# Performance work log

Measured on AMD Instinct MI355X. Metric: run time of the kernel, lower is better.

The kernel has to match this reference:

```python
import jax, jax.numpy as jnp
import numpy as np


def setup_inputs() -> dict:
    key = jax.random.key(0)
    k1, k2, k3, k4 = jax.random.split(key, 4)
    b, h, t, dim, topk = 16, 8, 196, 512, 49
    x = jax.random.normal(k1, (b, t, dim), dtype=jnp.float32)
    adj = jax.random.normal(k2, (b, h, t, t), dtype=jnp.float32)  # per-head routing logits
    Wqkv = jax.random.normal(k3, (dim, 3 * dim), dtype=jnp.float32) * 0.02
    Wv = jax.random.normal(k4, (dim, dim), dtype=jnp.float32) * 0.02
    return {"x": x, "adj": adj, "Wqkv": Wqkv, "Wv": Wv, "topk": topk}


def reference(x, adj, Wqkv, Wv, topk):
    b, t, dim = x.shape
    h = adj.shape[1]
    d = dim // h
    scale = dim ** (-0.5)  # note: full dim, matching source (self.scale = dim**-0.5)

    # qkv projection (stand-in for GIN conv_proj_qkv with nhid = 3*dim)
    qkv = (x @ Wqkv).reshape(b, t, h, 3 * d).transpose(0, 2, 1, 3)  # b h t 3d
    q, k, v = jnp.split(qkv, 3, axis=-1)  # each b h t d

    # TopkRouting: indices of top-k routing logits per (b, h, query-token)
    _, r_idx = jax.lax.top_k(adj, topk)  # b h t topk (r_weight unused: mul_weight='none')

    # KGather: irregular gather of concatenated k/v rows per query token
    kv = jnp.concatenate([k, v], axis=-1).reshape(b * h, t, 2 * d)
    idx = r_idx.reshape(b * h, t, topk)
    kv_sel = jax.vmap(lambda m, i: m[i])(kv, idx)          # (bh, t, topk, 2d)
    kv_sel = kv_sel.reshape(b, h, t, topk, 2 * d)
    k_sel, v_sel = jnp.split(kv_sel, 2, axis=-1)            # b h t topk d

    # small-window attention: each query attends to its topk gathered rows (w^2 = 1)
    attn = jax.nn.softmax(jnp.einsum('bhtd,bhtkd->bhtk', q * scale, k_sel), axis=-1)
    o = jnp.einsum('bhtk,bhtkd->bhtd', attn, v_sel)

    o = o.transpose(0, 2, 1, 3).reshape(b, t, dim)
    o = jax.nn.gelu(o, approximate=False)  # torch F.gelu default = exact erf
    return o @ Wv
```

## Files before the change

### kernel.cpp

```cpp
#include <hip/hip_runtime.h>
#include <hip/hip_bf16.h>
#include <cmath>

#define B_   16
#define H_   8
#define T_   196
#define DIM_ 512
#define DHEAD_ 64
#define TOPK_ 49
#define BT_  (B_ * T_)
#define BH_  (B_ * H_)

#define QB_OFF   0u
#define KB_OFF   1605632u
#define VT_OFF   3211264u
#define XB_OFF   5046272u
#define WQKVT_OFF 6651904u
#define WVT_OFF  7438336u
#define MASK_OFF 7700480u

typedef __bf16 bf16x8 __attribute__((ext_vector_type(8)));
typedef float f32x4 __attribute__((ext_vector_type(4)));

__device__ __forceinline__ unsigned short f2bf(float f) {
    union { float f; unsigned int u; } v; v.f = f;
    const unsigned int u = v.u;
    return (unsigned short)((u + 0x7FFFu + ((u >> 16) & 1u)) >> 16);
}

__device__ __forceinline__ unsigned int ordered_u32(float f) {
    int i = __float_as_int(f);
    return (i < 0) ? ~(unsigned int)i : ((unsigned int)i | 0x80000000u);
}

__global__ __launch_bounds__(256) void prep_route(const float* __restrict__ x,
                                                  const float* __restrict__ adj,
                                                  const float* __restrict__ Wqkv,
                                                  const float* __restrict__ Wv,
                                                  unsigned short* __restrict__ xb,
                                                  unsigned short* __restrict__ wqkvT,
                                                  unsigned short* __restrict__ wvT,
                                                  unsigned short* __restrict__ vT,
                                                  unsigned int* __restrict__ masks) {
    __shared__ unsigned short Tt[64][72];
    const int t = threadIdx.x;
    const int bid = blockIdx.x;

    if (bid < 6272) {
        const int lane = t & 63;
        const int wid = t >> 6;
        const int q = bid * 4 + wid;
        const float* arow = adj + (size_t)q * T_;

        const bool v3 = (lane < 4);
        unsigned int u[4];
        u[0] = ordered_u32(arow[lane]);
        u[1] = ordered_u32(arow[lane + 64]);
        u[2] = ordered_u32(arow[lane + 128]);
        u[3] = v3 ? ordered_u32(arow[lane + 192]) : 0u;

        unsigned int prefix = 0u, thr = 0u;
        int k = TOPK_, A = T_;
        for (int b = 31; b >= 0; --b) {
            int C1 = 0;
            C1 += __popcll(__ballot(((u[0] ^ prefix) >> b) == 1u));
            C1 += __popcll(__ballot(((u[1] ^ prefix) >> b) == 1u));
            C1 += __popcll(__ballot(((u[2] ^ prefix) >> b) == 1u));
            C1 += __popcll(__ballot(((u[3] ^ prefix) >> b) == 1u));
            if (C1 >= k) { prefix |= (1u << b); A = C1; }
            else { k -= C1; A -= C1; }

            if (k == A || k == 1) {
                const bool mx = (k == 1);
                unsigned int best = mx ? 0u : 0xFFFFFFFFu;
#pragma unroll
                for (int s = 0; s < 4; ++s) {
                    const bool valid = (s < 3) || v3;
                    const bool act = valid && (((u[s] ^ prefix) >> b) == 0u);
                    if (act) best = mx ? (u[s] > best ? u[s] : best)
                                       : (u[s] < best ? u[s] : best);
                }
#pragma unroll
                for (int off = 32; off >= 1; off >>= 1) {
                    const unsigned int o = __shfl_xor(best, off);
                    best = mx ? (o > best ? o : best) : (o < best ? o : best);
                }
                thr = best;
                break;
            }
            if (b == 0) thr = prefix;
        }

        const unsigned long long lmask = (1ull << lane) - 1ull;
        unsigned long long gm[4];
        int G = 0;
#pragma unroll
        for (int s = 0; s < 4; ++s) {
            const bool valid = (s < 3) || v3;
            gm[s] = __ballot(valid && (u[s] > thr));
            G += __popcll(gm[s]);
        }
        const int need = TOPK_ - G;
        int cum = 0;
        unsigned long long sb0 = 0, sb1 = 0, sb2 = 0, sb3 = 0;
#pragma unroll
        for (int s = 0; s < 4; ++s) {
            const bool valid = (s < 3) || v3;
            const bool e = valid && (u[s] == thr);
            const unsigned long long em = __ballot(e);
            const int rk = cum + __popcll(em & lmask);
            cum += __popcll(em);
            const unsigned long long sel = gm[s] | __ballot(e && (rk < need));
            if (s == 0) sb0 = sel; else if (s == 1) sb1 = sel;
            else if (s == 2) sb2 = sel; else sb3 = sel;
        }
        if (lane < 8) {
            const unsigned long long mv = (lane < 2) ? sb0 : (lane < 4) ? sb1
                                        : (lane < 6) ? sb2 : sb3;
            const unsigned int wd = (lane & 1) ? (unsigned int)(mv >> 32) : (unsigned int)mv;
            masks[(size_t)q * 8 + lane] = wd;
        }
        return;
    }

    if (bid < 7056) {
        const size_t base = ((size_t)(bid - 6272) * 256 + t) * 8;
        const float4 v0 = *(const float4*)&x[base];
        const float4 v1 = *(const float4*)&x[base + 4];
        uint4 pk;
        pk.x = (unsigned int)f2bf(v0.x) | ((unsigned int)f2bf(v0.y) << 16);
        pk.y = (unsigned int)f2bf(v0.z) | ((unsigned int)f2bf(v0.w) << 16);
        pk.z = (unsigned int)f2bf(v1.x) | ((unsigned int)f2bf(v1.y) << 16);
        pk.w = (unsigned int)f2bf(v1.z) | ((unsigned int)f2bf(v1.w) << 16);
        *(uint4*)&xb[base] = pk;
        return;
    }
    if (bid >= 7312) {
        const int e0 = (bid - 7312) * 8192 + t;
#pragma unroll
        for (int i = 0; i < 32; ++i) {
            const int e = e0 + i * 256;
            const int bh = e / 1792;
            const int rem = e - bh * 1792;
            const int d = rem / 28;
            const int tt = rem - d * 28;
            vT[(size_t)bh * (64 * 224) + (size_t)d * 224 + 196 + tt] = 0;
        }
        return;
    }

    const float* src;
    unsigned short* dst;
    int Cc, R, tx, ty;
    if (bid < 7248) {
        const int b = bid - 7056;
        src = Wqkv; dst = wqkvT; Cc = 1536; R = 512; tx = b % 24; ty = b / 24;
    } else {
        const int b = bid - 7248;
        src = Wv; dst = wvT; Cc = 512; R = 512; tx = b % 8; ty = b / 8;
    }
    const int c0 = tx * 64;
    const int r0 = ty * 64;

#pragma unroll
    for (int p = 0; p < 4; ++p) {
        const int r = (t >> 4) + 16 * p;
        const int cl = (t & 15) * 4;
        const float4 v = *(const float4*)&src[(size_t)(r0 + r) * Cc + c0 + cl];
        Tt[cl + 0][r] = f2bf(v.x);
        Tt[cl + 1][r] = f2bf(v.y);
        Tt[cl + 2][r] = f2bf(v.z);
        Tt[cl + 3][r] = f2bf(v.w);
    }
    __syncthreads();
#pragma unroll
    for (int p = 0; p < 2; ++p) {
        const int cc = (t >> 3) + 32 * p;
        const int ch = (t & 7) * 8;
        const uint4 v = *(const uint4*)&Tt[cc][ch];
        *(uint4*)&dst[(size_t)(c0 + cc) * R + r0 + ch] = v;
    }
}

template <int BN, int MODE, typename CT>
__global__ __launch_bounds__(256) void gemm_mfma(const unsigned short* __restrict__ A,
                                                 const unsigned short* __restrict__ Bt,
                                                 CT* __restrict__ C,
                                                 const int M, const int N, const int K) {
    constexpr int FN = BN / 32;
    __shared__ unsigned short As[64][56];
    __shared__ unsigned short Bs[BN][56];
    __shared__ unsigned short Cs[(MODE == 1) ? 64 * 132 : 4];

    const int tid = threadIdx.x;
    const int lane = tid & 63, wid = tid >> 6;
    const int wr = wid >> 1, wc = wid & 1;
    const int row0 = blockIdx.x * 64;
    const int col0 = blockIdx.y * BN;

    f32x4 acc[2][FN];
#pragma unroll
    for (int m = 0; m < 2; ++m)
#pragma unroll
        for (int n = 0; n < FN; ++n)
            acc[m][n] = (f32x4){0.0f, 0.0f, 0.0f, 0.0f};

    const int ar = tid >> 2;
    const int ac = (tid & 3) * 8;
    const int fr = lane & 15;
    const int fk = (lane >> 4) * 8;

    for (int k0 = 0; k0 < K; k0 += 32) {
        *(uint4*)&As[ar][ac] = *(const uint4*)&A[(size_t)(row0 + ar) * K + k0 + ac];
#pragma unroll
        for (int p = 0; p < BN / 64; ++p)
            *(uint4*)&Bs[p * 64 + ar][ac] =
                *(const uint4*)&Bt[(size_t)(col0 + p * 64 + ar) * K + k0 + ac];
        __syncthreads();

        bf16x8 af[2], bfv[FN];
#pragma unroll
        for (int m = 0; m < 2; ++m)
            af[m] = *(const bf16x8*)&As[wr * 32 + m * 16 + fr][fk];
#pragma unroll
        for (int n = 0; n < FN; ++n)
            bfv[n] = *(const bf16x8*)&Bs[wc * (BN / 2) + n * 16 + fr][fk];
#pragma unroll
        for (int m = 0; m < 2; ++m)
#pragma unroll
            for (int n = 0; n < FN; ++n)
                acc[m][n] = __builtin_amdgcn_mfma_f32_16x16x32_bf16(af[m], bfv[n], acc[m][n], 0, 0, 0);
        __syncthreads();
    }

    if (MODE == 0) {
#pragma unroll
        for (int m = 0; m < 2; ++m)
#pragma unroll
            for (int n = 0; n < FN; ++n)
#pragma unroll
                for (int i = 0; i < 4; ++i) {
                    const int row = row0 + wr * 32 + m * 16 + (lane >> 4) * 4 + i;
                    const int col = col0 + wc * (BN / 2) + n * 16 + (lane & 15);
                    C[(size_t)row * N + col] = (CT)acc[m][n][i];
                }
    } else {
#pragma unroll
        for (int m = 0; m < 2; ++m)
#pragma unroll
            for (int n = 0; n < FN; ++n)
#pragma unroll
                for (int i = 0; i < 4; ++i) {
                    const int rl = wr * 32 + m * 16 + (lane >> 4) * 4 + i;
                    const int cl = wc * (BN / 2) + n * 16 + (lane & 15);
                    Cs[rl * 132 + cl] = f2bf(acc[m][n][i]);
                }
        __syncthreads();

        unsigned short* ubase = (unsigned short*)C;
#pragma unroll
        for (int ch = 0; ch < BN / 64; ++ch) {
            const int abscol = col0 + ch * 64;
            const int which = (abscol >> 6) % 3;
            const int hh = abscol / 192;
            if (which < 2) {
                const int r = tid >> 2;
                const int co = (tid & 3) * 16;
                const int gr = row0 + r;
                const int bb = gr / T_;
                const int tt = gr - bb * T_;
                const uint2 a0 = *(const uint2*)&Cs[r * 132 + ch * 64 + co];
                const uint2 a1 = *(const uint2*)&Cs[r * 132 + ch * 64 + co + 4];
                const uint2 a2 = *(const uint2*)&Cs[r * 132 + ch * 64 + co + 8];
                const uint2 a3 = *(const uint2*)&Cs[r * 132 + ch * 64 + co + 12];
                unsigned short* dst = ubase + (size_t)which * KB_OFF +
                                      ((size_t)(bb * H_ + hh) * T_ + tt) * DHEAD_ + co;
                uint4 w0; w0.x = a0.x; w0.y = a0.y; w0.z = a1.x; w0.w = a1.y;
                uint4 w1; w1.x = a2.x; w1.y = a2.y; w1.z = a3.x; w1.w = a3.y;
                *(uint4*)&dst[0] = w0;
                *(uint4*)&dst[8] = w1;
            } else {
                const int d = tid >> 2;
                const int j0 = (tid & 3) * 16;
                union { unsigned short s[16]; uint2 v2[4]; } tmp;
#pragma unroll
                for (int j = 0; j < 16; ++j)
                    tmp.s[j] = Cs[(j0 + j) * 132 + ch * 64 + d];
                const int gr0 = row0 + j0;
                const int bb0 = gr0 / T_;
                const int bb1 = (gr0 + 15) / T_;
                if (bb0 == bb1) {
                    const int tt = gr0 - bb0 * T_;
                    unsigned short* dst = ubase + VT_OFF +
                                          (size_t)(bb0 * H_ + hh) * (64 * 224) +
                                          (size_t)d * 224 + tt;
                    *(uint2*)&dst[0]  = tmp.v2[0];
                    *(uint2*)&dst[4]  = tmp.v2[1];
                    *(uint2*)&dst[8]  = tmp.v2[2];
                    *(uint2*)&dst[12] = tmp.v2[3];
                } else {
#pragma unroll
                    for (int j = 0; j < 16; ++j) {
                        const int gr = gr0 + j;
                        const int bb = gr / T_;
                        const int tt = gr - bb * T_;
                        ubase[VT_OFF + (size_t)(bb * H_ + hh) * (64 * 224) +
                              (size_t)d * 224 + tt] = tmp.s[j];
                    }
                }
            }
        }
    }
}

__global__ __launch_bounds__(256) void attn_mfma(const unsigned short* __restrict__ qb,
                                                 const unsigned short* __restrict__ kb,
                                                 const unsigned short* __restrict__ vT,
                                                 const unsigned int* __restrict__ masks,
                                                 unsigned short* __restrict__ obuf) {
    __shared__ unsigned int mask_lds[64][8];
    __shared__ unsigned short P[64][232];

    const int lane = threadIdx.x & 63;
    const int w = threadIdx.x >> 6;
    const int qt = blockIdx.x;
    const int bh = blockIdx.y;
    const int bb = bh >> 3, hh = bh & 7;
    const int q0 = qt * 64;

    for (int it = threadIdx.x; it < 512; it += 256) {
        const int r = it >> 3, wd = it & 7;
        const int t = q0 + r;
        mask_lds[r][wd] = (t < T_) ? masks[((size_t)bh * T_ + t) * 8 + wd] : 0u;
    }
    *(unsigned long long*)&P[threadIdx.x >> 2][208 + (threadIdx.x & 3) * 4] = 0ull;
    __syncthreads();

    const int fr = lane & 15;
    const int fk8 = (lane >> 4) * 8;
    const unsigned short* qbh = qb + ((size_t)bh * T_ + q0 + w * 16) * DHEAD_;
    const unsigned short* kbh = kb + (size_t)bh * T_ * DHEAD_;

    bf16x8 aq0 = *(const bf16x8*)&qbh[fr * 64 + fk8];
    bf16x8 aq1 = *(const bf16x8*)&qbh[fr * 64 + 32 + fk8];

    f32x4 s[13];
#pragma unroll
    for (int c = 0; c < 13; ++c) s[c] = (f32x4){0.0f, 0.0f, 0.0f, 0.0f};
#pragma unroll
    for (int c = 0; c < 13; ++c) {
        const bf16x8 b0 = *(const bf16x8*)&kbh[(c * 16 + fr) * 64 + fk8];
        const bf16x8 b1 = *(const bf16x8*)&kbh[(c * 16 + fr) * 64 + 32 + fk8];
        s[c] = __builtin_amdgcn_mfma_f32_16x16x32_bf16(aq0, b0, s[c], 0, 0, 0);
        s[c] = __builtin_amdgcn_mfma_f32_16x16x32_bf16(aq1, b1, s[c], 0, 0, 0);
    }

    const float scale = 0.044194173824159216f;
    float l0 = 0, l1 = 0, l2 = 0, l3 = 0;
#pragma unroll
    for (int i = 0; i < 4; ++i) {
        const int rowl = w * 16 + (lane >> 4) * 4 + i;
        float li = 0.0f;
#pragma unroll
        for (int c = 0; c < 13; ++c) {
            const unsigned int mw = mask_lds[rowl][c >> 1];
            const bool sel = (mw >> (((c & 1) << 4) + fr)) & 1u;
            const float pv = sel ? __expf(s[c][i] * scale) : 0.0f;
            P[rowl][c * 16 + fr] = f2bf(pv);
            li += pv;
        }
        if (i == 0) l0 = li; else if (i == 1) l1 = li;
        else if (i == 2) l2 = li; else l3 = li;
    }
#pragma unroll
    for (int off = 8; off >= 1; off >>= 1) {
        l0 += __shfl_xor(l0, off);
        l1 += __shfl_xor(l1, off);
        l2 += __shfl_xor(l2, off);
        l3 += __shfl_xor(l3, off);
    }
    const float rl0 = 1.0f / l0, rl1 = 1.0f / l1, rl2 = 1.0f / l2, rl3 = 1.0f / l3;

    const unsigned short* vbh = vT + (size_t)bh * (64 * 224);
    f32x4 o[4];
#pragma unroll
    for (int n = 0; n < 4; ++n) o[n] = (f32x4){0.0f, 0.0f, 0.0f, 0.0f};
#pragma unroll
    for (int kk = 0; kk < 7; ++kk) {
        const bf16x8 ap = *(const bf16x8*)&P[w * 16 + fr][kk * 32 + fk8];
#pragma unroll
        for (int n = 0; n < 4; ++n) {
            const bf16x8 bv = *(const bf16x8*)&vbh[(n * 16 + fr) * 224 + kk * 32 + fk8];
            o[n] = __builtin_amdgcn_mfma_f32_16x16x32_bf16(ap, bv, o[n], 0, 0, 0);
        }
    }

#pragma unroll
    for (int i = 0; i < 4; ++i) {
        const float rl = (i == 0) ? rl0 : (i == 1) ? rl1 : (i == 2) ? rl2 : rl3;
        const int t = q0 + w * 16 + (lane >> 4) * 4 + i;
        if (t < T_) {
            unsigned short* orow = obuf + ((size_t)(bb * T_ + t)) * DIM_ + hh * DHEAD_;
#pragma unroll
            for (int n = 0; n < 4; ++n) {
                const float ov = o[n][i] * rl;
                const float g = 0.5f * ov * (1.0f + erff(ov * 0.70710678118654752f));
                orow[n * 16 + fr] = f2bf(g);
            }
        }
    }
}

extern "C" void kernel_launch(void* const* d_in, const int* in_sizes, int n_in,
                              void* d_out, int out_size, void* d_ws, size_t ws_size,
                              hipStream_t stream) {
    const float* x    = (const float*)d_in[0];
    const float* adj  = (const float*)d_in[1];
    const float* Wqkv = (const float*)d_in[2];
    const float* Wv   = (const float*)d_in[3];
    float* out = (float*)d_out;
    unsigned short* ub = (unsigned short*)d_ws;

    unsigned short* qb    = ub + QB_OFF;
    unsigned short* kb    = ub + KB_OFF;
    unsigned short* vT    = ub + VT_OFF;
    unsigned short* xb    = ub + XB_OFF;
    unsigned short* wqkvT = ub + WQKVT_OFF;
    unsigned short* wvT   = ub + WVT_OFF;
    unsigned int*   masks = (unsigned int*)(ub + MASK_OFF);

    prep_route<<<7340, 256, 0, stream>>>(x, adj, Wqkv, Wv, xb, wqkvT, wvT, vT, masks);

    dim3 g1(BT_ / 64, 1536 / 128);
    gemm_mfma<128, 1, unsigned short><<<g1, 256, 0, stream>>>(xb, wqkvT, ub, BT_, 3 * DIM_, DIM_);

    attn_mfma<<<dim3(4, BH_), 256, 0, stream>>>(qb, kb, vT, masks, xb);

    dim3 g2(BT_ / 64, DIM_ / 64);
    gemm_mfma<64, 0, float><<<g2, 256, 0, stream>>>(xb, wvT, out, BT_, DIM_, DIM_);
}
```

Before: 74.14 us.

## Fuse top-k routing into QKV GEMM grid, use direct LDS loads, shrink attention blocks

Moves the top-k routing, vT padding zeroing and Wv transpose out of the prep kernel and into extra blocks of the QKV GEMM launch. The independent routing work then runs alongside the GEMM instead of before it. The GEMM now stages tiles with global_load_lds (direct-to-LDS) and keeps its A/B/C buffers in a shared-memory union. The attention kernel goes from 256-thread blocks of 64 queries to 64-thread blocks of 16 queries, giving more blocks across the CUs. The risks are heavier grid scheduling, load imbalance between routing blocks and GEMM blocks, and the removal of LDS padding, which may cause bank conflicts.

```diff
diff --git a/kernel.cpp b/kernel.cpp
--- a/kernel.cpp
+++ b/kernel.cpp
@@ -33,98 +33,96 @@
     return (i < 0) ? ~(unsigned int)i : ((unsigned int)i | 0x80000000u);
 }
 
-__global__ __launch_bounds__(256) void prep_route(const float* __restrict__ x,
-                                                  const float* __restrict__ adj,
-                                                  const float* __restrict__ Wqkv,
-                                                  const float* __restrict__ Wv,
-                                                  unsigned short* __restrict__ xb,
-                                                  unsigned short* __restrict__ wqkvT,
-                                                  unsigned short* __restrict__ wvT,
-                                                  unsigned short* __restrict__ vT,
-                                                  unsigned int* __restrict__ masks) {
+__device__ __forceinline__ void gload16(const void* g, void* l) {
+    __builtin_amdgcn_global_load_lds(
+        (const __attribute__((address_space(1))) unsigned int*)g,
+        (__attribute__((address_space(3))) unsigned int*)l, 16, 0, 0);
+}
+
+__device__ __forceinline__ void route_topk_q(const float* __restrict__ adj,
+                                             unsigned int* __restrict__ masks,
+                                             const int q, const int lane) {
+    const float* arow = adj + (size_t)q * T_;
+    const bool v3 = (lane < 4);
+    unsigned int u[4];
+    u[0] = ordered_u32(arow[lane]);
+    u[1] = ordered_u32(arow[lane + 64]);
+    u[2] = ordered_u32(arow[lane + 128]);
+    u[3] = v3 ? ordered_u32(arow[lane + 192]) : 0u;
+
+    unsigned int prefix = 0u, thr = 0u;
+    int k = TOPK_, A = T_;
+    for (int b = 31; b >= 0; --b) {
+        int C1 = 0;
+        C1 += __popcll(__ballot(((u[0] ^ prefix) >> b) == 1u));
+        C1 += __popcll(__ballot(((u[1] ^ prefix) >> b) == 1u));
+        C1 += __popcll(__ballot(((u[2] ^ prefix) >> b) == 1u));
+        C1 += __popcll(__ballot(((u[3] ^ prefix) >> b) == 1u));
+        if (C1 >= k) { prefix |= (1u << b); A = C1; }
+        else { k -= C1; A -= C1; }
+
+        if (k == A || k == 1) {
+            const bool mx = (k == 1);
+            unsigned int best = mx ? 0u : 0xFFFFFFFFu;
+#pragma unroll
+            for (int s2 = 0; s2 < 4; ++s2) {
+                const bool valid = (s2 < 3) || v3;
+                const bool act = valid && (((u[s2] ^ prefix) >> b) == 0u);
+                if (act) best = mx ? (u[s2] > best ? u[s2] : best)
+                                   : (u[s2] < best ? u[s2] : best);
+            }
+#pragma unroll
+            for (int off = 32; off >= 1; off >>= 1) {
+                const unsigned int o = __shfl_xor(best, off);
+                best = mx ? (o > best ? o : best) : (o < best ? o : best);
+            }
+            thr = best;
+            break;
+        }
+        if (b == 0) thr = prefix;
+    }
+
+    const unsigned long long lmask = (1ull << lane) - 1ull;
+    unsigned long long gm[4];
+    int G = 0;
+#pragma unroll
+    for (int s2 = 0; s2 < 4; ++s2) {
+        const bool valid = (s2 < 3) || v3;
+        gm[s2] = __ballot(valid && (u[s2] > thr));
+        G += __popcll(gm[s2]);
+    }
+    const int need = TOPK_ - G;
+    int cum = 0;
+    unsigned long long sb0 = 0, sb1 = 0, sb2 = 0, sb3 = 0;
+#pragma unroll
+    for (int s2 = 0; s2 < 4; ++s2) {
+        const bool valid = (s2 < 3) || v3;
+        const bool e = valid && (u[s2] == thr);
+        const unsigned long long em = __ballot(e);
+        const int rk = cum + __popcll(em & lmask);
+        cum += __popcll(em);
+        const unsigned long long sel = gm[s2] | __ballot(e && (rk < need));
+        if (s2 == 0) sb0 = sel; else if (s2 == 1) sb1 = sel;
+        else if (s2 == 2) sb2 = sel; else sb3 = sel;
+    }
+    if (lane < 8) {
+        const unsigned long long mv = (lane < 2) ? sb0 : (lane < 4) ? sb1
+                                    : (lane < 6) ? sb2 : sb3;
+        const unsigned int wd = (lane & 1) ? (unsigned int)(mv >> 32) : (unsigned int)mv;
+        masks[(size_t)q * 8 + lane] = wd;
+    }
+}
+
+__global__ __launch_bounds__(256) void prep(const float* __restrict__ x,
+                                            const float* __restrict__ Wqkv,
+                                            unsigned short* __restrict__ xb,
+                                            unsigned short* __restrict__ wqkvT) {
     __shared__ unsigned short Tt[64][72];
     const int t = threadIdx.x;
     const int bid = blockIdx.x;
 
-    if (bid < 6272) {
-        const int lane = t & 63;
-        const int wid = t >> 6;
-        const int q = bid * 4 + wid;
-        const float* arow = adj + (size_t)q * T_;
-
-        const bool v3 = (lane < 4);
-        unsigned int u[4];
-        u[0] = ordered_u32(arow[lane]);
-        u[1] = ordered_u32(arow[lane + 64]);
-        u[2] = ordered_u32(arow[lane + 128]);
-        u[3] = v3 ? ordered_u32(arow[lane + 192]) : 0u;
-
-        unsigned int prefix = 0u, thr = 0u;
-        int k = TOPK_, A = T_;
-        for (int b = 31; b >= 0; --b) {
-            int C1 = 0;
-            C1 += __popcll(__ballot(((u[0] ^ prefix) >> b) == 1u));
-            C1 += __popcll(__ballot(((u[1] ^ prefix) >> b) == 1u));
-            C1 += __popcll(__ballot(((u[2] ^ prefix) >> b) == 1u));
-            C1 += __popcll(__ballot(((u[3] ^ prefix) >> b) == 1u));
-            if (C1 >= k) { prefix |= (1u << b); A = C1; }
-            else { k -= C1; A -= C1; }
-
-            if (k == A || k == 1) {
-                const bool mx = (k == 1);
-                unsigned int best = mx ? 0u : 0xFFFFFFFFu;
-#pragma unroll
-                for (int s = 0; s < 4; ++s) {
-                    const bool valid = (s < 3) || v3;
-                    const bool act = valid && (((u[s] ^ prefix) >> b) == 0u);
-                    if (act) best = mx ? (u[s] > best ? u[s] : best)
-                                       : (u[s] < best ? u[s] : best);
-                }
-#pragma unroll
-                for (int off = 32; off >= 1; off >>= 1) {
-                    const unsigned int o = __shfl_xor(best, off);
-                    best = mx ? (o > best ? o : best) : (o < best ? o : best);
-                }
-                thr = best;
-                break;
-            }
-            if (b == 0) thr = prefix;
-        }
-
-        const unsigned long long lmask = (1ull << lane) - 1ull;
-        unsigned long long gm[4];
-        int G = 0;
-#pragma unroll
-        for (int s = 0; s < 4; ++s) {
-            const bool valid = (s < 3) || v3;
-            gm[s] = __ballot(valid && (u[s] > thr));
-            G += __popcll(gm[s]);
-        }
-        const int need = TOPK_ - G;
-        int cum = 0;
-        unsigned long long sb0 = 0, sb1 = 0, sb2 = 0, sb3 = 0;
-#pragma unroll
-        for (int s = 0; s < 4; ++s) {
-            const bool valid = (s < 3) || v3;
-            const bool e = valid && (u[s] == thr);
-            const unsigned long long em = __ballot(e);
-            const int rk = cum + __popcll(em & lmask);
-            cum += __popcll(em);
-            const unsigned long long sel = gm[s] | __ballot(e && (rk < need));
-            if (s == 0) sb0 = sel; else if (s == 1) sb1 = sel;
-            else if (s == 2) sb2 = sel; else sb3 = sel;
-        }
-        if (lane < 8) {
-            const unsigned long long mv = (lane < 2) ? sb0 : (lane < 4) ? sb1
-                                        : (lane < 6) ? sb2 : sb3;
-            const unsigned int wd = (lane & 1) ? (unsigned int)(mv >> 32) : (unsigned int)mv;
-            masks[(size_t)q * 8 + lane] = wd;
-        }
-        return;
-    }
-
-    if (bid < 7056) {
-        const size_t base = ((size_t)(bid - 6272) * 256 + t) * 8;
+    if (bid < 784) {
+        const size_t base = ((size_t)bid * 256 + t) * 8;
         const float4 v0 = *(const float4*)&x[base];
         const float4 v1 = *(const float4*)&x[base + 4];
         uint4 pk;
@@ -135,38 +133,15 @@
         *(uint4*)&xb[base] = pk;
         return;
     }
-    if (bid >= 7312) {
-        const int e0 = (bid - 7312) * 8192 + t;
-#pragma unroll
-        for (int i = 0; i < 32; ++i) {
-            const int e = e0 + i * 256;
-            const int bh = e / 1792;
-            const int rem = e - bh * 1792;
-            const int d = rem / 28;
-            const int tt = rem - d * 28;
-            vT[(size_t)bh * (64 * 224) + (size_t)d * 224 + 196 + tt] = 0;
-        }
-        return;
-    }
-
-    const float* src;
-    unsigned short* dst;
-    int Cc, R, tx, ty;
-    if (bid < 7248) {
-        const int b = bid - 7056;
-        src = Wqkv; dst = wqkvT; Cc = 1536; R = 512; tx = b % 24; ty = b / 24;
-    } else {
-        const int b = bid - 7248;
-        src = Wv; dst = wvT; Cc = 512; R = 512; tx = b % 8; ty = b / 8;
-    }
-    const int c0 = tx * 64;
-    const int r0 = ty * 64;
-
+
+    const int b = bid - 784;
+    const int tx = b % 24, ty = b / 24;
+    const int c0 = tx * 64, r0 = ty * 64;
 #pragma unroll
     for (int p = 0; p < 4; ++p) {
         const int r = (t >> 4) + 16 * p;
         const int cl = (t & 15) * 4;
-        const float4 v = *(const float4*)&src[(size_t)(r0 + r) * Cc + c0 + cl];
+        const float4 v = *(const float4*)&Wqkv[(size_t)(r0 + r) * 1536 + c0 + cl];
         Tt[cl + 0][r] = f2bf(v.x);
         Tt[cl + 1][r] = f2bf(v.y);
         Tt[cl + 2][r] = f2bf(v.z);
@@ -177,26 +152,83 @@
     for (int p = 0; p < 2; ++p) {
         const int cc = (t >> 3) + 32 * p;
         const int ch = (t & 7) * 8;
-        const uint4 v = *(const uint4*)&Tt[cc][ch];
-        *(uint4*)&dst[(size_t)(c0 + cc) * R + r0 + ch] = v;
-    }
-}
-
-template <int BN, int MODE, typename CT>
+        *(uint4*)&wqkvT[(size_t)(c0 + cc) * 512 + r0 + ch] = *(const uint4*)&Tt[cc][ch];
+    }
+}
+
+template <int BN, int MODE, int FUSE, typename CT>
 __global__ __launch_bounds__(256) void gemm_mfma(const unsigned short* __restrict__ A,
                                                  const unsigned short* __restrict__ Bt,
                                                  CT* __restrict__ C,
-                                                 const int M, const int N, const int K) {
+                                                 const int M, const int N, const int K,
+                                                 const float* __restrict__ adj,
+                                                 unsigned int* __restrict__ masks,
+                                                 unsigned short* __restrict__ vT,
+                                                 const float* __restrict__ Wv,
+                                                 unsigned short* __restrict__ wvT) {
     constexpr int FN = BN / 32;
-    __shared__ unsigned short As[64][56];
-    __shared__ unsigned short Bs[BN][56];
-    __shared__ unsigned short Cs[(MODE == 1) ? 64 * 132 : 4];
+    constexpr int CSZ = (MODE == 1) ? 64 * 132 : 1;
+    struct ABt { unsigned short A[64][32]; unsigned short B[BN][32]; };
+    __shared__ union {
+        ABt ab;
+        unsigned short Cs[CSZ];
+        unsigned short Tt[FUSE ? 64 : 1][72];
+    } sm;
 
     const int tid = threadIdx.x;
     const int lane = tid & 63, wid = tid >> 6;
+    const int mt = M >> 6;
+    const int nGemm = mt * (N / BN);
+    const int bid = blockIdx.x;
+
+    if constexpr (FUSE) {
+        if (bid >= nGemm) {
+            const int rid = bid - nGemm;
+            if (rid < 6272) {
+                route_topk_q(adj, masks, rid * 4 + wid, lane);
+            } else if (rid < 6300) {
+                const int e0 = (rid - 6272) * 8192 + tid;
+#pragma unroll
+                for (int i = 0; i < 32; ++i) {
+                    const int e = e0 + i * 256;
+                    const int bh = e / 1792;
+                    const int rem = e - bh * 1792;
+                    const int d = rem / 28;
+                    const int tt = rem - d * 28;
+                    vT[(size_t)bh * (64 * 224) + (size_t)d * 224 + 196 + tt] = 0;
+                }
+            } else {
+                const int b = rid - 6300;
+                const int tx = b & 7, ty = b >> 3;
+                const int c0 = tx * 64, r0 = ty * 64;
+#pragma unroll
+                for (int p = 0; p < 4; ++p) {
+                    const int r = (tid >> 4) + 16 * p;
+                    const int cl = (tid & 15) * 4;
+                    const float4 v = *(const float4*)&Wv[(size_t)(r0 + r) * 512 + c0 + cl];
+                    sm.Tt[cl + 0][r] = f2bf(v.x);
+                    sm.Tt[cl + 1][r] = f2bf(v.y);
+                    sm.Tt[cl + 2][r] = f2bf(v.z);
+                    sm.Tt[cl + 3][r] = f2bf(v.w);
+                }
+                __syncthreads();
+#pragma unroll
+                for (int p = 0; p < 2; ++p) {
+                    const int cc = (tid >> 3) + 32 * p;
+                    const int ch = (tid & 7) * 8;
+                    *(uint4*)&wvT[(size_t)(c0 + cc) * 512 + r0 + ch] =
+                        *(const uint4*)&sm.Tt[cc][ch];
+                }
+            }
+            return;
+        }
+    }
+
+    const int bx = bid % mt;
+    const int by = bid / mt;
+    const int row0 = bx * 64;
+    const int col0 = by * BN;
     const int wr = wid >> 1, wc = wid & 1;
-    const int row0 = blockIdx.x * 64;
-    const int col0 = blockIdx.y * BN;
 
     f32x4 acc[2][FN];
 #pragma unroll
@@ -205,26 +237,32 @@
         for (int n = 0; n < FN; ++n)
             acc[m][n] = (f32x4){0.0f, 0.0f, 0.0f, 0.0f};
 
-    const int ar = tid >> 2;
-    const int ac = (tid & 3) * 8;
+    const int srow = lane >> 2;
+    const int scol = (lane & 3) * 8;
+    const unsigned short* aSrc = A + (size_t)(row0 + wid * 16 + srow) * K + scol;
+    const unsigned short* bSrc = Bt + (size_t)(col0 + wid * 16 + srow) * K + scol;
+    const unsigned short* bSrc2 = bSrc + (size_t)64 * K;
+    unsigned short* ldsA = &sm.ab.A[wid * 16][0];
+    unsigned short* ldsB = &sm.ab.B[wid * 16][0];
+    unsigned short* ldsB2 = &sm.ab.B[(BN == 128 ? 64 : 0) + wid * 16][0];
+
     const int fr = lane & 15;
-    const int fk = (lane >> 4) * 8;
+    const int fk8 = (lane >> 4) * 8;
 
     for (int k0 = 0; k0 < K; k0 += 32) {
-        *(uint4*)&As[ar][ac] = *(const uint4*)&A[(size_t)(row0 + ar) * K + k0 + ac];
-#pragma unroll
-        for (int p = 0; p < BN / 64; ++p)
-            *(uint4*)&Bs[p * 64 + ar][ac] =
-                *(const uint4*)&Bt[(size_t)(col0 + p * 64 + ar) * K + k0 + ac];
+        gload16(aSrc, ldsA);
+        gload16(bSrc, ldsB);
+        if constexpr (BN == 128) gload16(bSrc2, ldsB2);
+        aSrc += 32; bSrc += 32; bSrc2 += 32;
         __syncthreads();
 
         bf16x8 af[2], bfv[FN];
 #pragma unroll
         for (int m = 0; m < 2; ++m)
-            af[m] = *(const bf16x8*)&As[wr * 32 + m * 16 + fr][fk];
+            af[m] = *(const bf16x8*)&sm.ab.A[wr * 32 + m * 16 + fr][fk8];
 #pragma unroll
         for (int n = 0; n < FN; ++n)
-            bfv[n] = *(const bf16x8*)&Bs[wc * (BN / 2) + n * 16 + fr][fk];
+            bfv[n] = *(const bf16x8*)&sm.ab.B[wc * (BN / 2) + n * 16 + fr][fk8];
 #pragma unroll
         for (int m = 0; m < 2; ++m)
 #pragma unroll
@@ -233,7 +271,7 @@
         __syncthreads();
     }
 
-    if (MODE == 0) {
+    if constexpr (MODE == 0) {
 #pragma unroll
         for (int m = 0; m < 2; ++m)
 #pragma unroll
@@ -253,7 +291,7 @@
                 for (int i = 0; i < 4; ++i) {
                     const int rl = wr * 32 + m * 16 + (lane >> 4) * 4 + i;
                     const int cl = wc * (BN / 2) + n * 16 + (lane & 15);
-                    Cs[rl * 132 + cl] = f2bf(acc[m][n][i]);
+                    sm.Cs[rl * 132 + cl] = f2bf(acc[m][n][i]);
                 }
         __syncthreads();
 
@@ -269,10 +307,10 @@
                 const int gr = row0 + r;
                 const int bb = gr / T_;
                 const int tt = gr - bb * T_;
-                const uint2 a0 = *(const uint2*)&Cs[r * 132 + ch * 64 + co];
-                const uint2 a1 = *(const uint2*)&Cs[r * 132 + ch * 64 + co + 4];
-                const uint2 a2 = *(const uint2*)&Cs[r * 132 + ch * 64 + co + 8];
-                const uint2 a3 = *(const uint2*)&Cs[r * 132 + ch * 64 + co + 12];
+                const uint2 a0 = *(const uint2*)&sm.Cs[r * 132 + ch * 64 + co];
+                const uint2 a1 = *(const uint2*)&sm.Cs[r * 132 + ch * 64 + co + 4];
+                const uint2 a2 = *(const uint2*)&sm.Cs[r * 132 + ch * 64 + co + 8];
+                const uint2 a3 = *(const uint2*)&sm.Cs[r * 132 + ch * 64 + co + 12];
                 unsigned short* dst = ubase + (size_t)which * KB_OFF +
                                       ((size_t)(bb * H_ + hh) * T_ + tt) * DHEAD_ + co;
                 uint4 w0; w0.x = a0.x; w0.y = a0.y; w0.z = a1.x; w0.w = a1.y;
@@ -285,7 +323,7 @@
                 union { unsigned short s[16]; uint2 v2[4]; } tmp;
 #pragma unroll
                 for (int j = 0; j < 16; ++j)
-                    tmp.s[j] = Cs[(j0 + j) * 132 + ch * 64 + d];
+                    tmp.s[j] = sm.Cs[(j0 + j) * 132 + ch * 64 + d];
                 const int gr0 = row0 + j0;
                 const int bb0 = gr0 / T_;
                 const int bb1 = (gr0 + 15) / T_;
@@ -313,36 +351,37 @@
     }
 }
 
-__global__ __launch_bounds__(256) void attn_mfma(const unsigned short* __restrict__ qb,
-                                                 const unsigned short* __restrict__ kb,
-                                                 const unsigned short* __restrict__ vT,
-                                                 const unsigned int* __restrict__ masks,
-                                                 unsigned short* __restrict__ obuf) {
-    __shared__ unsigned int mask_lds[64][8];
-    __shared__ unsigned short P[64][232];
-
-    const int lane = threadIdx.x & 63;
-    const int w = threadIdx.x >> 6;
+__global__ __launch_bounds__(64) void attn_mfma(const unsigned short* __restrict__ qb,
+                                                const unsigned short* __restrict__ kb,
+                                                const unsigned short* __restrict__ vT,
+                                                const unsigned int* __restrict__ masks,
+                                                unsigned short* __restrict__ obuf) {
+    __shared__ unsigned int mask_lds[16][8];
+    __shared__ unsigned short P[16][232];
+
+    const int lane = threadIdx.x;
     const int qt = blockIdx.x;
     const int bh = blockIdx.y;
     const int bb = bh >> 3, hh = bh & 7;
-    const int q0 = qt * 64;
-
-    for (int it = threadIdx.x; it < 512; it += 256) {
-        const int r = it >> 3, wd = it & 7;
+    const int q0 = qt * 16;
+
+#pragma unroll
+    for (int s2 = 0; s2 < 2; ++s2) {
+        const int e = lane + s2 * 64;
+        const int r = e >> 3, wd = e & 7;
         const int t = q0 + r;
         mask_lds[r][wd] = (t < T_) ? masks[((size_t)bh * T_ + t) * 8 + wd] : 0u;
     }
-    *(unsigned long long*)&P[threadIdx.x >> 2][208 + (threadIdx.x & 3) * 4] = 0ull;
+    *(unsigned long long*)&P[lane >> 2][208 + (lane & 3) * 4] = 0ull;
     __syncthreads();
 
     const int fr = lane & 15;
     const int fk8 = (lane >> 4) * 8;
-    const unsigned short* qbh = qb + ((size_t)bh * T_ + q0 + w * 16) * DHEAD_;
+    const unsigned short* qbh = qb + ((size_t)bh * T_ + q0) * DHEAD_;
     const unsigned short* kbh = kb + (size_t)bh * T_ * DHEAD_;
 
-    bf16x8 aq0 = *(const bf16x8*)&qbh[fr * 64 + fk8];
-    bf16x8 aq1 = *(const bf16x8*)&qbh[fr * 64 + 32 + fk8];
+    const bf16x8 aq0 = *(const bf16x8*)&qbh[fr * 64 + fk8];
+    const bf16x8 aq1 = *(const bf16x8*)&qbh[fr * 64 + 32 + fk8];
 
     f32x4 s[13];
 #pragma unroll
@@ -359,7 +398,7 @@
     float l0 = 0, l1 = 0, l2 = 0, l3 = 0;
 #pragma unroll
     for (int i = 0; i < 4; ++i) {
-        const int rowl = w * 16 + (lane >> 4) * 4 + i;
+        const int rowl = (lane >> 4) * 4 + i;
         float li = 0.0f;
 #pragma unroll
         for (int c = 0; c < 13; ++c) {
@@ -387,7 +426,7 @@
     for (int n = 0; n < 4; ++n) o[n] = (f32x4){0.0f, 0.0f, 0.0f, 0.0f};
 #pragma unroll
     for (int kk = 0; kk < 7; ++kk) {
-        const bf16x8 ap = *(const bf16x8*)&P[w * 16 + fr][kk * 32 + fk8];
+        const bf16x8 ap = *(const bf16x8*)&P[fr][kk * 32 + fk8];
 #pragma unroll
         for (int n = 0; n < 4; ++n) {
             const bf16x8 bv = *(const bf16x8*)&vbh[(n * 16 + fr) * 224 + kk * 32 + fk8];
@@ -398,7 +437,7 @@
 #pragma unroll
     for (int i = 0; i < 4; ++i) {
         const float rl = (i == 0) ? rl0 : (i == 1) ? rl1 : (i == 2) ? rl2 : rl3;
-        const int t = q0 + w * 16 + (lane >> 4) * 4 + i;
+        const int t = q0 + (lane >> 4) * 4 + i;
         if (t < T_) {
             unsigned short* orow = obuf + ((size_t)(bb * T_ + t)) * DIM_ + hh * DHEAD_;
 #pragma unroll
@@ -429,13 +468,13 @@
     unsigned short* wvT   = ub + WVT_OFF;
     unsigned int*   masks = (unsigned int*)(ub + MASK_OFF);
 
-    prep_route<<<7340, 256, 0, stream>>>(x, adj, Wqkv, Wv, xb, wqkvT, wvT, vT, masks);
-
-    dim3 g1(BT_ / 64, 1536 / 128);
-    gemm_mfma<128, 1, unsigned short><<<g1, 256, 0, stream>>>(xb, wqkvT, ub, BT_, 3 * DIM_, DIM_);
-
-    attn_mfma<<<dim3(4, BH_), 256, 0, stream>>>(qb, kb, vT, masks, xb);
-
-    dim3 g2(BT_ / 64, DIM_ / 64);
-    gemm_mfma<64, 0, float><<<g2, 256, 0, stream>>>(xb, wvT, out, BT_, DIM_, DIM_);
-}
+    prep<<<976, 256, 0, stream>>>(x, Wqkv, xb, wqkvT);
+
+    gemm_mfma<128, 1, 1, unsigned short><<<6952, 256, 0, stream>>>(
+        xb, wqkvT, ub, BT_, 3 * DIM_, DIM_, adj, masks, vT, Wv, wvT);
+
+    attn_mfma<<<dim3(13, BH_), 64, 0, stream>>>(qb, kb, vT, masks, xb);
+
+    gemm_mfma<64, 0, 0, float><<<392, 256, 0, stream>>>(
+        xb, wvT, out, BT_, DIM_, DIM_, nullptr, nullptr, nullptr, nullptr, nullptr);
+}
```

Result: faster. 67.76 us (-8.6%).
